# Optimization experiments

Hardware: AMD Instinct MI355X
Metric: run time of the kernel (lower is better)

The kernel has to match this reference:

```python
import jax, jax.numpy as jnp
import numpy as np
from jax import lax

B, M = 16384, 200            # flattened batch*time, tokens per observation
NUM_LAYERS, OW, OH = 22, 11, 11
HIDDEN = 512

_MAX_VEC = jnp.maximum(jnp.array([9.0, 1.0, 1.0, 10.0, 3.0, 254.0, 1.0, 1.0, 235.0, 8.0,
                                  9.0, 250.0, 29.0, 1.0, 1.0, 8.0, 1.0, 1.0, 6.0, 3.0,
                                  1.0, 2.0], dtype=jnp.float32), 1.0)


def setup_inputs() -> dict:
    key = jax.random.key(0)
    ks = jax.random.split(key, 10)
    init = lambda k, shp, std: (jax.random.normal(k, shp, dtype=jnp.float32) * std)
    observations = jax.random.randint(ks[0], (B, M, 3), 0, 255, dtype=jnp.int32)
    return {
        "observations": observations,
        # CNN: Conv2d(22,128,5,s=3) -> Conv2d(128,128,3,s=1) -> Linear(128,256)
        "conv1_w": init(ks[1], (128, NUM_LAYERS, 5, 5), 0.04), "conv1_b": jnp.zeros((128,), jnp.float32),
        "conv2_w": init(ks[2], (128, 128, 3, 3), 0.03),        "conv2_b": jnp.zeros((128,), jnp.float32),
        "fc_w": init(ks[3], (256, 128), 0.08),                 "fc_b": jnp.zeros((256,), jnp.float32),
        # self encoder Linear(22,256)
        "self_w": init(ks[4], (256, NUM_LAYERS), 0.2),         "self_b": jnp.zeros((256,), jnp.float32),
        # actor heads (nvec=[9,10]) and value head
        "actor0_w": init(ks[5], (9, HIDDEN), 0.01),            "actor0_b": jnp.zeros((9,), jnp.float32),
        "actor1_w": init(ks[6], (10, HIDDEN), 0.01),           "actor1_b": jnp.zeros((10,), jnp.float32),
        "value_w": init(ks[7], (1, HIDDEN), 1.0 / np.sqrt(HIDDEN)), "value_b": jnp.zeros((1,), jnp.float32),
    }


def reference(observations, conv1_w, conv1_b, conv2_w, conv2_b, fc_w, fc_b,
              self_w, self_b, actor0_w, actor0_b, actor1_w, actor1_b, value_w, value_b):
    # --- token parsing + scatter into dense grid ---
    obs = jnp.where(observations == 255, 0, observations)          # [B, M, 3]
    coords = obs[..., 0]
    x = (coords >> 4) & 15
    y = coords & 15
    atr = obs[..., 1]
    vals = obs[..., 2].astype(jnp.float32)
    valid = (coords != 255) & (x < OW) & (y < OH) & (atr < NUM_LAYERS)
    atr_s = jnp.where(valid, atr, NUM_LAYERS)                      # route invalid OOB -> dropped
    b_idx = jnp.broadcast_to(jnp.arange(B)[:, None], atr.shape)
    box = jnp.zeros((B, NUM_LAYERS, OW, OH), jnp.float32)
    box = box.at[b_idx, atr_s, x, y].set(vals, mode='drop')
    feat = box / (_MAX_VEC[None, :, None, None] + 1e-8)            # [B, 22, 11, 11]

    # --- self encoder on center cell ---
    self_f = jax.nn.relu(feat[:, :, 5, 5] @ self_w.T + self_b)     # [B, 256]

    # --- CNN trunk ---
    h = lax.conv_general_dilated(feat, conv1_w, (3, 3), 'VALID')   # [B, 128, 3, 3]
    h = jax.nn.relu(h + conv1_b[None, :, None, None])
    h = lax.conv_general_dilated(h, conv2_w, (1, 1), 'VALID')      # [B, 128, 1, 1]
    h = jax.nn.relu(h + conv2_b[None, :, None, None]).reshape(B, -1)
    cnn_f = jax.nn.relu(h @ fc_w.T + fc_b)                         # [B, 256]

    hidden = jnp.concatenate([self_f, cnn_f], axis=1)              # [B, 512]

    # --- heads ---
    a0 = hidden @ actor0_w.T + actor0_b                            # [B, 9]
    a1 = hidden @ actor1_w.T + actor1_b                            # [B, 10]
    v = hidden @ value_w.T + value_b                               # [B, 1]
    return a0, a1, v
```

## Files before the change

### kernel.cpp

```cpp
#include <hip/hip_runtime.h>
#include <stdint.h>

typedef __bf16 bf16x8 __attribute__((ext_vector_type(8)));
typedef float  f32x4  __attribute__((ext_vector_type(4)));

#define B_TOT 16384
#define GS    8
#define MB2   32

#define OFF_W1T   0u
#define OFF_W2B   141312u
#define OFF_FCB   436224u
#define OFF_WH    501760u
#define OFF_BH    534528u
#define OFF_SWB   534656u
#define OFF_SELFV 551040u
#define OFF_H1    1599616u

__device__ const float d_maxv[22] = {
  9.f,1.f,1.f,10.f,3.f,254.f,1.f,1.f,235.f,8.f,
  9.f,250.f,29.f,1.f,1.f,8.f,1.f,1.f,6.f,3.f,1.f,2.f };

static __device__ __forceinline__ short f2bf(float f){
  union { float f; uint32_t u; } c; c.f = f;
  uint32_t r = (c.u + 0x7FFFu + ((c.u >> 16) & 1u)) >> 16;
  return (short)r;
}
static __device__ __forceinline__ float bf2f(short s){
  union { uint32_t u; float f; } c; c.u = ((uint32_t)(uint16_t)s) << 16;
  return c.f;
}
static __device__ __forceinline__ uint32_t cvtpk(float lo, float hi){
  uint32_t pk;
  asm("v_cvt_pk_bf16_f32 %0, %1, %2" : "=v"(pk) : "v"(lo), "v"(hi));
  return pk;
}
static __device__ __forceinline__ int swz(int row, int k, int stride){
  return row * stride + ((((k >> 3) ^ (row & 7)) << 3) | (k & 7));
}
static __device__ __forceinline__ void gld16(const void* g, void* l){
  __builtin_amdgcn_global_load_lds(
      (const __attribute__((address_space(1))) void*)g,
      (__attribute__((address_space(3))) void*)l, 16, 0, 0);
}
static __device__ __forceinline__ void wavesync(){
  asm volatile("s_waitcnt lgkmcnt(0)" ::: "memory");
  __builtin_amdgcn_wave_barrier();
}

__global__ __launch_bounds__(256) void k_prep(
    const float* __restrict__ c1w, const float* __restrict__ c2w,
    const float* __restrict__ fcw, const float* __restrict__ a0w,
    const float* __restrict__ a1w, const float* __restrict__ vw,
    const float* __restrict__ a0b, const float* __restrict__ a1b,
    const float* __restrict__ vb,  const float* __restrict__ selfw,
    short* __restrict__ w1t, short* __restrict__ w2b, short* __restrict__ fcb,
    short* __restrict__ wh, float* __restrict__ bh, short* __restrict__ swB)
{
  int i = blockIdx.x * 256 + threadIdx.x;
  if (i < 70400) {
    int r = i >> 7, oc = i & 127;
    w1t[i] = f2bf(c1w[oc * 550 + r]);
  }
  i -= 70400;
  if (i >= 0 && i < 147456) {
    int oc = i / 1152, k = i - oc * 1152;
    int pos = k >> 7, ic = k & 127;
    w2b[i] = f2bf(c2w[oc * 1152 + ic * 9 + pos]);
  }
  i -= 147456;
  if (i >= 0 && i < 32768) fcb[i] = f2bf(fcw[i]);
  i -= 32768;
  if (i >= 0 && i < 16384) {
    int j = i >> 9, k = i & 511;
    float v = 0.f;
    if (j < 9) v = a0w[j * 512 + k];
    else if (j < 19) v = a1w[(j - 9) * 512 + k];
    else if (j == 19) v = vw[k];
    wh[i] = f2bf(v);
  }
  i -= 16384;
  if (i >= 0 && i < 32) {
    float v = 0.f;
    if (i < 9) v = a0b[i]; else if (i < 19) v = a1b[i - 9]; else if (i == 19) v = vb[0];
    bh[i] = v;
  }
  i -= 32;
  if (i >= 0 && i < 8192) {
    int o = i >> 5, l = i & 31;
    swB[i] = (l < 22) ? f2bf(selfw[o * 22 + l]) : (short)0;
  }
}

__global__ __launch_bounds__(512, 8) void k_scatter(
    const int* __restrict__ obs, const float* __restrict__ c1b,
    const short* __restrict__ w1t,
    short* __restrict__ selfvB, short* __restrict__ h1)
{
  __shared__ uint32_t nzl[GS * 64];
  __shared__ uint2    eP2[GS * 144];
  __shared__ uint32_t cnt[GS];
  __shared__ uint32_t pcnt[GS * 9];
  __shared__ float selfv[GS * 24];
  __shared__ float invS[22];

  const int tid = threadIdx.x, wid = tid >> 6, lane = tid & 63;
  const int b = blockIdx.x * GS + wid;

  if (lane == 0) cnt[wid] = 0u;
  if (lane < 9)  pcnt[wid * 9 + lane] = 0u;
  if (lane < 24) selfv[wid * 24 + lane] = 0.f;
  if (tid < 22) invS[tid] = 1.0f / (d_maxv[tid] + 1e-8f);
  __syncthreads();

  {
    const int* base = obs + (size_t)b * 600;
    #pragma unroll
    for (int k = 0; k < 4; ++k) {
      int m = lane + (k << 6);
      if (m < 200) {
        int c = base[m * 3], a = base[m * 3 + 1], v = base[m * 3 + 2];
        c = (c == 255) ? 0 : c;  a = (a == 255) ? 0 : a;  v = (v == 255) ? 0 : v;
        int x = (c >> 4) & 15, y = c & 15;
        if (x < 11 && y < 11 && a < 22) {
          uint32_t cell = (uint32_t)(a * 121 + x * 11 + y);
          uint32_t idx = atomicAdd(&cnt[wid], 1u);
          if (idx < 64u)
            nzl[wid * 64 + idx] = ((uint32_t)m << 20) | (cell << 8) | (uint32_t)v;
        }
      }
    }
  }
  wavesync();

  {
    uint32_t n = cnt[wid]; if (n > 64u) n = 64u;
    for (uint32_t i = lane; i < n; i += 64) {
      uint32_t e = nzl[wid * 64 + i];
      uint32_t cell = (e >> 8) & 0xFFFu;
      uint32_t best = e;
      for (uint32_t j = 0; j < n; ++j) {
        uint32_t ej = nzl[wid * 64 + j];
        if ((((ej >> 8) & 0xFFFu) == cell) && ej > best) best = ej;
      }
      if (best == e && (e & 255u) != 0u) {
        uint32_t v8 = e & 255u;
        uint32_t l = cell / 121u, rem = cell - l * 121u;
        uint32_t x = rem / 11u, y = rem - x * 11u;
        float vf = (float)v8 * invS[l];
        if (rem == 60u)
          selfv[wid * 24 + l] = vf;
        #pragma unroll
        for (int ox = 0; ox < 3; ++ox) {
          int kx = (int)x - 3 * ox; if (kx < 0 || kx > 4) continue;
          #pragma unroll
          for (int oy = 0; oy < 3; ++oy) {
            int ky = (int)y - 3 * oy; if (ky < 0 || ky > 4) continue;
            uint32_t r = l * 25u + (uint32_t)kx * 5u + (uint32_t)ky;
            uint32_t p = (uint32_t)(ox * 3 + oy);
            uint32_t s = atomicAdd(&pcnt[wid * 9 + p], 1u);
            if (s < 16u) {
              uint2 pr; pr.x = r; pr.y = __float_as_uint(vf);
              eP2[wid * 144 + p * 16 + s] = pr;
            }
          }
        }
      }
    }
  }
  wavesync();

  if (lane < 9) {
    uint32_t m = pcnt[wid * 9 + lane];
    if (m > 16u) m = 16u;
    if (m & 1u) { uint2 z; z.x = 0u; z.y = 0u; eP2[wid * 144 + lane * 16 + m] = z; ++m; }
    pcnt[wid * 9 + lane] = m;
  }
  wavesync();

  if (lane < 16) {
    int l0 = lane * 2;
    float v0 = (l0     < 22) ? selfv[wid * 24 + l0]     : 0.f;
    float v1 = (l0 + 1 < 22) ? selfv[wid * 24 + l0 + 1] : 0.f;
    *(uint32_t*)(selfvB + (size_t)b * 32 + l0) = cvtpk(v0, v1);
  }

  {
    const int oc0 = 2 * lane;
    const float bz0 = c1b[oc0], bz1 = c1b[oc0 + 1];
    uint32_t* dst = (uint32_t*)h1 + (size_t)b * 576 + lane;
    const uint2* bkt = &eP2[wid * 144];

    #pragma unroll
    for (int p = 0; p < 9; ++p) {
      float a0 = bz0, a1 = bz1;
      const int n = (int)pcnt[wid * 9 + p];
      for (int i = 0; i < n; i += 2) {
        uint2 e0 = bkt[p * 16 + i];
        uint2 e1 = bkt[p * 16 + i + 1];
        int r0 = __builtin_amdgcn_readfirstlane((int)e0.x);
        int r1 = __builtin_amdgcn_readfirstlane((int)e1.x);
        uint32_t w0 = *(const uint32_t*)(const void*)&w1t[r0 * 128 + oc0];
        uint32_t w1 = *(const uint32_t*)(const void*)&w1t[r1 * 128 + oc0];
        float v0 = __uint_as_float(e0.y);
        float v1 = __uint_as_float(e1.y);
        a0 += v0 * bf2f((short)(w0 & 0xFFFFu)) + v1 * bf2f((short)(w1 & 0xFFFFu));
        a1 += v0 * bf2f((short)(w0 >> 16))     + v1 * bf2f((short)(w1 >> 16));
      }
      dst[p * 64] = cvtpk(fmaxf(a0, 0.f), fmaxf(a1, 0.f));
    }
  }
}

__global__ __launch_bounds__(512, 4) void k_mlp(
    const short* __restrict__ h1, const short* __restrict__ selfvB,
    const short* __restrict__ w2b, const short* __restrict__ fcb,
    const short* __restrict__ wh,  const short* __restrict__ swB,
    const float* __restrict__ c2b, const float* __restrict__ fcbias,
    const float* __restrict__ selfb, const float* __restrict__ bh,
    float* __restrict__ out)
{
  __shared__ __align__(16) short smem[20480];

  const int tid  = threadIdx.x, wid = tid >> 6, lane = tid & 63;
  const int l15 = lane & 15, kg = lane >> 4;
  const int wr = wid & 1, wc = wid >> 1;
  const int rowA = wr * 16 + l15;
  const size_t b0 = (size_t)blockIdx.x * MB2;
  const f32x4 z4 = {0.f, 0.f, 0.f, 0.f};

  const int sub = lane >> 3, pch = lane & 7;
  const int ocj0 = (wid * 2) * 8 + sub, ocj1 = (wid * 2 + 1) * 8 + sub;
  const short* gB0 = w2b + (size_t)ocj0 * 1152 + ((pch ^ (ocj0 & 7)) << 3);
  const short* gB1 = w2b + (size_t)ocj1 * 1152 + ((pch ^ (ocj1 & 7)) << 3);
  const int dB0 = 2048 + (wid * 2) * 512, dB1 = 2048 + (wid * 2 + 1) * 512;
  const int rowi = ((wid >= 4) ? (wid - 4) : 0) * 8 + sub;
  const short* gA = h1 + (b0 + rowi) * 1152 + ((pch ^ (rowi & 7)) << 3);
  const int dA = ((wid >= 4) ? (wid - 4) : 0) * 512;

  f32x4 acc[2] = {z4, z4};
  {
    gld16(gB0, &smem[dB0]); gld16(gB1, &smem[dB1]);
    if (wid >= 4) gld16(gA, &smem[dA]);
  }
  for (int t = 0; t < 18; ++t) {
    const int cb = (t & 1) * 10240;
    if (t < 17) {
      const int nb = 10240 - cb;
      const int ko = (t + 1) * 64;
      gld16(gB0 + ko, &smem[nb + dB0]); gld16(gB1 + ko, &smem[nb + dB1]);
      if (wid >= 4) {
        gld16(gA + ko, &smem[nb + dA]);
        asm volatile("s_waitcnt vmcnt(3)" ::: "memory");
      } else {
        asm volatile("s_waitcnt vmcnt(2)" ::: "memory");
      }
    } else {
      asm volatile("s_waitcnt vmcnt(0)" ::: "memory");
    }
    __builtin_amdgcn_sched_barrier(0);
    __builtin_amdgcn_s_barrier();
    __builtin_amdgcn_sched_barrier(0);
    #pragma unroll
    for (int ks = 0; ks < 2; ++ks) {
      int kq = ks * 4 + kg;
      bf16x8 a = *(const bf16x8*)(const void*)
                 &smem[cb + rowA * 64 + ((kq ^ (rowA & 7)) << 3)];
      #pragma unroll
      for (int nf = 0; nf < 2; ++nf) {
        int oc = wc * 32 + nf * 16 + l15;
        bf16x8 bv = *(const bf16x8*)(const void*)
                    &smem[cb + 2048 + oc * 64 + ((kq ^ (oc & 7)) << 3)];
        acc[nf] = __builtin_amdgcn_mfma_f32_16x16x32_bf16(a, bv, acc[nf], 0, 0, 0);
      }
    }
    __builtin_amdgcn_sched_barrier(0);
    __builtin_amdgcn_s_barrier();
  }
  #pragma unroll
  for (int nf = 0; nf < 2; ++nf) {
    int col = wc * 32 + nf * 16 + l15;
    float bias = c2b[col];
    #pragma unroll
    for (int rr = 0; rr < 4; ++rr) {
      int row = wr * 16 + kg * 4 + rr;
      smem[swz(row, col, 128)] = f2bf(fmaxf(acc[nf][rr] + bias, 0.f));
    }
  }
  __syncthreads();

  {
    f32x4 fca[4] = {z4, z4, z4, z4};
    #pragma unroll
    for (int kk = 0; kk < 4; ++kk) {
      int k = kk * 32 + kg * 8;
      bf16x8 a = *(const bf16x8*)(const void*)&smem[swz(rowA, k, 128)];
      #pragma unroll
      for (int nf = 0; nf < 4; ++nf) {
        int col = wc * 64 + nf * 16 + l15;
        bf16x8 bv = *(const bf16x8*)(const void*)(fcb + (size_t)col * 128 + k);
        fca[nf] = __builtin_amdgcn_mfma_f32_16x16x32_bf16(a, bv, fca[nf], 0, 0, 0);
      }
    }
    #pragma unroll
    for (int nf = 0; nf < 4; ++nf) {
      int col = wc * 64 + nf * 16 + l15;
      float bias = fcbias[col];
      #pragma unroll
      for (int rr = 0; rr < 4; ++rr) {
        int row = wr * 16 + kg * 4 + rr;
        smem[4096 + swz(row, col, 256)] = f2bf(fmaxf(fca[nf][rr] + bias, 0.f));
      }
    }
  }
  {
    f32x4 sa[4] = {z4, z4, z4, z4};
    bf16x8 a = *(const bf16x8*)(const void*)
               (selfvB + (b0 + (size_t)rowA) * 32 + kg * 8);
    #pragma unroll
    for (int nf = 0; nf < 4; ++nf) {
      int col = wc * 64 + nf * 16 + l15;
      bf16x8 bv = *(const bf16x8*)(const void*)(swB + (size_t)col * 32 + kg * 8);
      sa[nf] = __builtin_amdgcn_mfma_f32_16x16x32_bf16(a, bv, sa[nf], 0, 0, 0);
    }
    #pragma unroll
    for (int nf = 0; nf < 4; ++nf) {
      int col = wc * 64 + nf * 16 + l15;
      float bias = selfb[col];
      #pragma unroll
      for (int rr = 0; rr < 4; ++rr) {
        int row = wr * 16 + kg * 4 + rr;
        smem[12288 + swz(row, col, 256)] = f2bf(fmaxf(sa[nf][rr] + bias, 0.f));
      }
    }
  }
  __syncthreads();

  {
    float* hacc = (float*)smem;
    const int kh = (wid >> 1) & 1, nh = wid >> 2;
    const int ncol = nh * 16 + l15;
    f32x4 ha = z4;
    #pragma unroll
    for (int kk = 0; kk < 8; ++kk) {
      int kl = kk * 32 + kg * 8;
      bf16x8 a;
      if (kh == 0) a = *(const bf16x8*)(const void*)&smem[12288 + swz(rowA, kl, 256)];
      else         a = *(const bf16x8*)(const void*)&smem[4096  + swz(rowA, kl, 256)];
      bf16x8 bv = *(const bf16x8*)(const void*)(wh + (size_t)ncol * 512 + kh * 256 + kl);
      ha = __builtin_amdgcn_mfma_f32_16x16x32_bf16(a, bv, ha, 0, 0, 0);
    }
    #pragma unroll
    for (int rr = 0; rr < 4; ++rr) {
      int row = wr * 16 + kg * 4 + rr;
      hacc[kh * 1024 + row * 32 + ncol] = ha[rr];
    }
  }
  __syncthreads();

  {
    const float* hacc = (const float*)smem;
    #pragma unroll
    for (int q = 0; q < 2; ++q) {
      int i = q * 512 + tid;
      int row = i >> 5, colh = i & 31;
      float v = hacc[i] + hacc[1024 + i] + bh[colh];
      int gr = (int)b0 + row;
      if (colh < 9)        out[gr * 9 + colh] = v;
      else if (colh < 19)  out[147456 + gr * 10 + (colh - 9)] = v;
      else if (colh == 19) out[311296 + gr] = v;
    }
  }
}

extern "C" void kernel_launch(void* const* d_in, const int* in_sizes, int n_in,
                              void* d_out, int out_size, void* d_ws, size_t ws_size,
                              hipStream_t stream)
{
  const int*   obs = (const int*)  d_in[0];
  const float* c1w = (const float*)d_in[1];
  const float* c1b = (const float*)d_in[2];
  const float* c2w = (const float*)d_in[3];
  const float* c2b = (const float*)d_in[4];
  const float* fcw = (const float*)d_in[5];
  const float* fcbv= (const float*)d_in[6];
  const float* sw  = (const float*)d_in[7];
  const float* sb  = (const float*)d_in[8];
  const float* a0w = (const float*)d_in[9];
  const float* a0b = (const float*)d_in[10];
  const float* a1w = (const float*)d_in[11];
  const float* a1b = (const float*)d_in[12];
  const float* vw  = (const float*)d_in[13];
  const float* vb  = (const float*)d_in[14];

  char* ws = (char*)d_ws;
  short* w1t    = (short*)(ws + OFF_W1T);
  short* w2b    = (short*)(ws + OFF_W2B);
  short* fcb    = (short*)(ws + OFF_FCB);
  short* wh     = (short*)(ws + OFF_WH);
  float* bh     = (float*)(ws + OFF_BH);
  short* swB    = (short*)(ws + OFF_SWB);
  short* selfvB = (short*)(ws + OFF_SELFV);
  short* h1     = (short*)(ws + OFF_H1);
  float* out    = (float*)d_out;

  k_prep<<<dim3(1076), dim3(256), 0, stream>>>(c1w, c2w, fcw, a0w, a1w, vw,
                                               a0b, a1b, vb, sw,
                                               w1t, w2b, fcb, wh, bh, swB);
  k_scatter<<<dim3(B_TOT / GS), dim3(512), 0, stream>>>(obs, c1b, w1t, selfvB, h1);
  k_mlp<<<dim3(B_TOT / MB2), dim3(512), 0, stream>>>(h1, selfvB, w2b, fcb, wh, swB,
                                                     c2b, fcbv, sb, bh, out);
}
```

Before: 57.01 us.

## Move conv1 computation into MLP kernel from compact token buckets

The scatter kernel becomes a token kernel that writes only compact per-position bucket entries (packed row index, layer and value) plus counts, not the dense bf16 conv1 activations. The MLP kernel loads these buckets, computes conv1 per position on the fly into an LDS A-tile, and feeds it straight into the conv2 MFMA loop. This removes the global round trip of h1, which is about 2.3 KB per sample. In exchange it adds gather work and a per-row ALU phase inside the GEMM pipeline, caps buckets at 12 entries instead of 16, and halves the scatter group size.

```diff
diff --git a/kernel.cpp b/kernel.cpp
--- a/kernel.cpp
+++ b/kernel.cpp
@@ -5,7 +5,7 @@
 typedef float  f32x4  __attribute__((ext_vector_type(4)));
 
 #define B_TOT 16384
-#define GS    8
+#define GS    4
 #define MB2   32
 
 #define OFF_W1T   0u
@@ -15,7 +15,8 @@
 #define OFF_BH    534528u
 #define OFF_SWB   534656u
 #define OFF_SELFV 551040u
-#define OFF_H1    1599616u
+#define OFF_PCG   1599616u
+#define OFF_ENT   2189440u
 
 __device__ const float d_maxv[22] = {
   9.f,1.f,1.f,10.f,3.f,254.f,1.f,1.f,235.f,8.f,
@@ -92,13 +93,13 @@
   }
 }
 
-__global__ __launch_bounds__(512, 8) void k_scatter(
-    const int* __restrict__ obs, const float* __restrict__ c1b,
-    const short* __restrict__ w1t,
-    short* __restrict__ selfvB, short* __restrict__ h1)
+__global__ __launch_bounds__(256) void k_tok(
+    const int* __restrict__ obs,
+    short* __restrict__ selfvB, uint32_t* __restrict__ entG,
+    uint32_t* __restrict__ pcntG)
 {
   __shared__ uint32_t nzl[GS * 64];
-  __shared__ uint2    eP2[GS * 144];
+  __shared__ uint32_t bkt[GS * 108];
   __shared__ uint32_t cnt[GS];
   __shared__ uint32_t pcnt[GS * 9];
   __shared__ float selfv[GS * 24];
@@ -110,6 +111,7 @@
   if (lane == 0) cnt[wid] = 0u;
   if (lane < 9)  pcnt[wid * 9 + lane] = 0u;
   if (lane < 24) selfv[wid * 24 + lane] = 0.f;
+  for (int i = lane; i < 108; i += 64) bkt[wid * 108 + i] = 0u;
   if (tid < 22) invS[tid] = 1.0f / (d_maxv[tid] + 1e-8f);
   __syncthreads();
 
@@ -147,9 +149,8 @@
         uint32_t v8 = e & 255u;
         uint32_t l = cell / 121u, rem = cell - l * 121u;
         uint32_t x = rem / 11u, y = rem - x * 11u;
-        float vf = (float)v8 * invS[l];
         if (rem == 60u)
-          selfv[wid * 24 + l] = vf;
+          selfv[wid * 24 + l] = (float)v8 * invS[l];
         #pragma unroll
         for (int ox = 0; ox < 3; ++ox) {
           int kx = (int)x - 3 * ox; if (kx < 0 || kx > 4) continue;
@@ -159,22 +160,12 @@
             uint32_t r = l * 25u + (uint32_t)kx * 5u + (uint32_t)ky;
             uint32_t p = (uint32_t)(ox * 3 + oy);
             uint32_t s = atomicAdd(&pcnt[wid * 9 + p], 1u);
-            if (s < 16u) {
-              uint2 pr; pr.x = r; pr.y = __float_as_uint(vf);
-              eP2[wid * 144 + p * 16 + s] = pr;
-            }
+            if (s < 12u)
+              bkt[wid * 108 + p * 12 + s] = (r << 13) | (l << 8) | v8;
           }
         }
       }
     }
-  }
-  wavesync();
-
-  if (lane < 9) {
-    uint32_t m = pcnt[wid * 9 + lane];
-    if (m > 16u) m = 16u;
-    if (m & 1u) { uint2 z; z.x = 0u; z.y = 0u; eP2[wid * 144 + lane * 16 + m] = z; ++m; }
-    pcnt[wid * 9 + lane] = m;
   }
   wavesync();
 
@@ -184,43 +175,27 @@
     float v1 = (l0 + 1 < 22) ? selfv[wid * 24 + l0 + 1] : 0.f;
     *(uint32_t*)(selfvB + (size_t)b * 32 + l0) = cvtpk(v0, v1);
   }
-
-  {
-    const int oc0 = 2 * lane;
-    const float bz0 = c1b[oc0], bz1 = c1b[oc0 + 1];
-    uint32_t* dst = (uint32_t*)h1 + (size_t)b * 576 + lane;
-    const uint2* bkt = &eP2[wid * 144];
-
-    #pragma unroll
-    for (int p = 0; p < 9; ++p) {
-      float a0 = bz0, a1 = bz1;
-      const int n = (int)pcnt[wid * 9 + p];
-      for (int i = 0; i < n; i += 2) {
-        uint2 e0 = bkt[p * 16 + i];
-        uint2 e1 = bkt[p * 16 + i + 1];
-        int r0 = __builtin_amdgcn_readfirstlane((int)e0.x);
-        int r1 = __builtin_amdgcn_readfirstlane((int)e1.x);
-        uint32_t w0 = *(const uint32_t*)(const void*)&w1t[r0 * 128 + oc0];
-        uint32_t w1 = *(const uint32_t*)(const void*)&w1t[r1 * 128 + oc0];
-        float v0 = __uint_as_float(e0.y);
-        float v1 = __uint_as_float(e1.y);
-        a0 += v0 * bf2f((short)(w0 & 0xFFFFu)) + v1 * bf2f((short)(w1 & 0xFFFFu));
-        a1 += v0 * bf2f((short)(w0 >> 16))     + v1 * bf2f((short)(w1 >> 16));
-      }
-      dst[p * 64] = cvtpk(fmaxf(a0, 0.f), fmaxf(a1, 0.f));
-    }
+  for (int i = lane; i < 108; i += 64) entG[(size_t)b * 108 + i] = bkt[wid * 108 + i];
+  if (lane < 9) {
+    uint32_t m = pcnt[wid * 9 + lane];
+    pcntG[(size_t)b * 9 + lane] = (m > 12u) ? 12u : m;
   }
 }
 
 __global__ __launch_bounds__(512, 4) void k_mlp(
-    const short* __restrict__ h1, const short* __restrict__ selfvB,
+    const uint32_t* __restrict__ entG, const uint32_t* __restrict__ pcntG,
+    const short* __restrict__ selfvB, const short* __restrict__ w1t,
     const short* __restrict__ w2b, const short* __restrict__ fcb,
     const short* __restrict__ wh,  const short* __restrict__ swB,
-    const float* __restrict__ c2b, const float* __restrict__ fcbias,
-    const float* __restrict__ selfb, const float* __restrict__ bh,
-    float* __restrict__ out)
+    const float* __restrict__ c1b, const float* __restrict__ c2b,
+    const float* __restrict__ fcbias, const float* __restrict__ selfb,
+    const float* __restrict__ bh, float* __restrict__ out)
 {
-  __shared__ __align__(16) short smem[20480];
+  __shared__ __align__(16) short smem[28032];
+  uint32_t* tokS  = (uint32_t*)(smem + 20480);
+  uint32_t* pcntS = (uint32_t*)(smem + 27392);
+  float*    invL  = (float*)(smem + 27968);
+  short*    Atile = smem + 16384;
 
   const int tid  = threadIdx.x, wid = tid >> 6, lane = tid & 63;
   const int l15 = lane & 15, kg = lane >> 4;
@@ -229,34 +204,69 @@
   const size_t b0 = (size_t)blockIdx.x * MB2;
   const f32x4 z4 = {0.f, 0.f, 0.f, 0.f};
 
+  const int cb1 = tid >> 4;
+  const int icg = tid & 15;
+  const int ic0 = icg * 8;
+
+  {
+    const int4* src = (const int4*)(entG + b0 * 108);
+    int4* dst = (int4*)tokS;
+    for (int i = tid; i < 864; i += 512) dst[i] = src[i];
+  }
+  if (tid < 288) pcntS[tid] = pcntG[b0 * 9 + tid];
+  if (tid < 22) invL[tid] = 1.0f / (d_maxv[tid] + 1e-8f);
+
+  float bz[8];
+  #pragma unroll
+  for (int j = 0; j < 8; ++j) bz[j] = c1b[ic0 + j];
+
   const int sub = lane >> 3, pch = lane & 7;
   const int ocj0 = (wid * 2) * 8 + sub, ocj1 = (wid * 2 + 1) * 8 + sub;
   const short* gB0 = w2b + (size_t)ocj0 * 1152 + ((pch ^ (ocj0 & 7)) << 3);
   const short* gB1 = w2b + (size_t)ocj1 * 1152 + ((pch ^ (ocj1 & 7)) << 3);
-  const int dB0 = 2048 + (wid * 2) * 512, dB1 = 2048 + (wid * 2 + 1) * 512;
-  const int rowi = ((wid >= 4) ? (wid - 4) : 0) * 8 + sub;
-  const short* gA = h1 + (b0 + rowi) * 1152 + ((pch ^ (rowi & 7)) << 3);
-  const int dA = ((wid >= 4) ? (wid - 4) : 0) * 512;
+  const int dB0 = (wid * 2) * 512, dB1 = (wid * 2 + 1) * 512;
+
+  gld16(gB0, &smem[dB0]); gld16(gB1, &smem[dB1]);
+  __syncthreads();
 
   f32x4 acc[2] = {z4, z4};
-  {
-    gld16(gB0, &smem[dB0]); gld16(gB1, &smem[dB1]);
-    if (wid >= 4) gld16(gA, &smem[dA]);
-  }
   for (int t = 0; t < 18; ++t) {
-    const int cb = (t & 1) * 10240;
+    if ((t & 1) == 0) {
+      const int p = t >> 1;
+      float a8[8];
+      #pragma unroll
+      for (int j = 0; j < 8; ++j) a8[j] = bz[j];
+      const int n = (int)pcntS[cb1 * 9 + p];
+      for (int i = 0; i < n; ++i) {
+        uint32_t e = tokS[cb1 * 108 + p * 12 + i];
+        int r = (int)(e >> 13);
+        float vf = (float)(e & 255u) * invL[(e >> 8) & 31u];
+        const uint32_t* wp = (const uint32_t*)(const void*)&w1t[r * 128 + ic0];
+        uint32_t w0 = wp[0], w1 = wp[1], w2 = wp[2], w3 = wp[3];
+        a8[0] += vf * bf2f((short)(w0 & 0xFFFFu));
+        a8[1] += vf * bf2f((short)(w0 >> 16));
+        a8[2] += vf * bf2f((short)(w1 & 0xFFFFu));
+        a8[3] += vf * bf2f((short)(w1 >> 16));
+        a8[4] += vf * bf2f((short)(w2 & 0xFFFFu));
+        a8[5] += vf * bf2f((short)(w2 >> 16));
+        a8[6] += vf * bf2f((short)(w3 & 0xFFFFu));
+        a8[7] += vf * bf2f((short)(w3 >> 16));
+      }
+      uint32_t* ad = (uint32_t*)(void*)&Atile[swz(cb1, ic0, 128)];
+      ad[0] = cvtpk(fmaxf(a8[0], 0.f), fmaxf(a8[1], 0.f));
+      ad[1] = cvtpk(fmaxf(a8[2], 0.f), fmaxf(a8[3], 0.f));
+      ad[2] = cvtpk(fmaxf(a8[4], 0.f), fmaxf(a8[5], 0.f));
+      ad[3] = cvtpk(fmaxf(a8[6], 0.f), fmaxf(a8[7], 0.f));
+    }
+    const int cbB = (t & 1) * 8192;
     if (t < 17) {
-      const int nb = 10240 - cb;
+      const int nbB = 8192 - cbB;
       const int ko = (t + 1) * 64;
-      gld16(gB0 + ko, &smem[nb + dB0]); gld16(gB1 + ko, &smem[nb + dB1]);
-      if (wid >= 4) {
-        gld16(gA + ko, &smem[nb + dA]);
-        asm volatile("s_waitcnt vmcnt(3)" ::: "memory");
-      } else {
-        asm volatile("s_waitcnt vmcnt(2)" ::: "memory");
-      }
+      gld16(gB0 + ko, &smem[nbB + dB0]);
+      gld16(gB1 + ko, &smem[nbB + dB1]);
+      asm volatile("s_waitcnt vmcnt(2) lgkmcnt(0)" ::: "memory");
     } else {
-      asm volatile("s_waitcnt vmcnt(0)" ::: "memory");
+      asm volatile("s_waitcnt vmcnt(0) lgkmcnt(0)" ::: "memory");
     }
     __builtin_amdgcn_sched_barrier(0);
     __builtin_amdgcn_s_barrier();
@@ -264,13 +274,13 @@
     #pragma unroll
     for (int ks = 0; ks < 2; ++ks) {
       int kq = ks * 4 + kg;
-      bf16x8 a = *(const bf16x8*)(const void*)
-                 &smem[cb + rowA * 64 + ((kq ^ (rowA & 7)) << 3)];
+      int icA = (t & 1) * 64 + kq * 8;
+      bf16x8 a = *(const bf16x8*)(const void*)&Atile[swz(rowA, icA, 128)];
       #pragma unroll
       for (int nf = 0; nf < 2; ++nf) {
         int oc = wc * 32 + nf * 16 + l15;
         bf16x8 bv = *(const bf16x8*)(const void*)
-                    &smem[cb + 2048 + oc * 64 + ((kq ^ (oc & 7)) << 3)];
+                    &smem[cbB + oc * 64 + ((kq ^ (oc & 7)) << 3)];
         acc[nf] = __builtin_amdgcn_mfma_f32_16x16x32_bf16(a, bv, acc[nf], 0, 0, 0);
       }
     }
@@ -401,13 +411,15 @@
   float* bh     = (float*)(ws + OFF_BH);
   short* swB    = (short*)(ws + OFF_SWB);
   short* selfvB = (short*)(ws + OFF_SELFV);
-  short* h1     = (short*)(ws + OFF_H1);
+  uint32_t* pcG = (uint32_t*)(ws + OFF_PCG);
+  uint32_t* enG = (uint32_t*)(ws + OFF_ENT);
   float* out    = (float*)d_out;
 
   k_prep<<<dim3(1076), dim3(256), 0, stream>>>(c1w, c2w, fcw, a0w, a1w, vw,
                                                a0b, a1b, vb, sw,
                                                w1t, w2b, fcb, wh, bh, swB);
-  k_scatter<<<dim3(B_TOT / GS), dim3(512), 0, stream>>>(obs, c1b, w1t, selfvB, h1);
-  k_mlp<<<dim3(B_TOT / MB2), dim3(512), 0, stream>>>(h1, selfvB, w2b, fcb, wh, swB,
-                                                     c2b, fcbv, sb, bh, out);
-}
+  k_tok<<<dim3(B_TOT / GS), dim3(256), 0, stream>>>(obs, selfvB, enG, pcG);
+  k_mlp<<<dim3(B_TOT / MB2), dim3(512), 0, stream>>>(enG, pcG, selfvB, w1t, w2b,
+                                                     fcb, wh, swB, c1b, c2b,
+                                                     fcbv, sb, bh, out);
+}
```

Result: slower. 58.25 us (+2.2%).
